# Performance work log

Hardware: AMD Instinct MI355X
Metric: run time of the kernel (lower is better)

The kernel has to match this reference:

```python
import jax, jax.numpy as jnp
import numpy as np

EMBED_DIM = 768
NUM_HEADS = 12
HEAD_DIM = EMBED_DIM // NUM_HEADS


def setup_inputs() -> dict:
    key = jax.random.key(0)
    ks = jax.random.split(key, 9)
    B, N, D = 8, 1024, EMBED_DIM
    s = 1.0 / np.sqrt(D)
    x = jax.random.normal(ks[0], (B, N, D), dtype=jnp.float32)
    Wq = jax.random.normal(ks[1], (D, D), dtype=jnp.float32) * s
    bq = jnp.zeros((D,), dtype=jnp.float32)
    Wk = jax.random.normal(ks[2], (D, D), dtype=jnp.float32) * s
    bk = jnp.zeros((D,), dtype=jnp.float32)
    Wv = jax.random.normal(ks[3], (D, D), dtype=jnp.float32) * s
    bv = jnp.zeros((D,), dtype=jnp.float32)
    Wo = jax.random.normal(ks[4], (D, D), dtype=jnp.float32) * s
    bo = jnp.zeros((D,), dtype=jnp.float32)
    return {"x": x, "Wq": Wq, "bq": bq, "Wk": Wk, "bk": bk,
            "Wv": Wv, "bv": bv, "Wo": Wo, "bo": bo}


def reference(x, Wq, bq, Wk, bk, Wv, bv, Wo, bo):
    B, N, D = x.shape
    H, Hd = NUM_HEADS, HEAD_DIM
    # torch Linear: y = x @ W.T + b
    q = (x @ Wq.T + bq).reshape(B, N, H, Hd).transpose(0, 2, 1, 3)  # [B,H,N,Hd]
    k = (x @ Wk.T + bk).reshape(B, N, H, Hd).transpose(0, 2, 1, 3)
    v = (x @ Wv.T + bv).reshape(B, N, H, Hd).transpose(0, 2, 1, 3)
    # NOTE: original scales by embed_dim**-0.5 (not head_dim)
    scale = jnp.asarray(D, x.dtype) ** -0.5
    scores = jnp.einsum('bhnd,bhmd->bhnm', q, k) * scale  # [B,H,N,N]
    attn = jax.nn.softmax(scores, axis=-1)
    out = jnp.einsum('bhnm,bhmd->bhnd', attn, v)  # dropout: identity in eval
    out = out.transpose(0, 2, 1, 3).reshape(B, N, D)
    return out @ Wo.T + bo
```

## Files before the change

kernel.cpp:

```cpp
#include <hip/hip_runtime.h>
#include <math.h>


typedef __bf16 bf16x8 __attribute__((ext_vector_type(8)));
typedef float  f32x4  __attribute__((ext_vector_type(4)));
typedef unsigned u32x2 __attribute__((ext_vector_type(2)));
typedef unsigned u32x4 __attribute__((ext_vector_type(4)));
typedef unsigned short ushort_t;

__device__ __forceinline__ unsigned short f2bf(float f) {
    unsigned u = __float_as_uint(f);
    u += 0x7fffu + ((u >> 16) & 1u);
    return (unsigned short)(u >> 16);
}
__device__ __forceinline__ unsigned pk16(unsigned short lo, unsigned short hi) {
    return (unsigned)lo | ((unsigned)hi << 16);
}

#define GLL16(g, l)                                                                        \
    __builtin_amdgcn_global_load_lds((const __attribute__((address_space(1))) void*)(g),   \
                                     (__attribute__((address_space(3))) void*)(l), 16, 0, 0)

__global__ __launch_bounds__(256)
void cast_all(const float* __restrict__ x,
              const float* __restrict__ w0, const float* __restrict__ w1,
              const float* __restrict__ w2, const float* __restrict__ w3,
              ushort_t* __restrict__ xb, ushort_t* __restrict__ wb0,
              ushort_t* __restrict__ wb1, ushort_t* __restrict__ wb2,
              ushort_t* __restrict__ wb3)
{
    const int y = blockIdx.y;
    const float* s; ushort_t* d; int n;
    switch (y) {
        case 0:  s = x;  d = xb;  n = 8192 * 768; break;
        case 1:  s = w0; d = wb0; n = 768 * 768;  break;
        case 2:  s = w1; d = wb1; n = 768 * 768;  break;
        case 3:  s = w2; d = wb2; n = 768 * 768;  break;
        default: s = w3; d = wb3; n = 768 * 768;  break;
    }
    const int i = (blockIdx.x * 256 + threadIdx.x) * 8;
    if (i >= n) return;
    const float4 f0 = *(const float4*)(s + i);
    const float4 f1 = *(const float4*)(s + i + 4);
    ushort4 p0, p1;
    p0.x = f2bf(f0.x); p0.y = f2bf(f0.y); p0.z = f2bf(f0.z); p0.w = f2bf(f0.w);
    p1.x = f2bf(f1.x); p1.y = f2bf(f1.y); p1.z = f2bf(f1.z); p1.w = f2bf(f1.w);
    *(ushort4*)(d + i)     = p0;
    *(ushort4*)(d + i + 4) = p1;
}

__device__ __forceinline__ void gemm_core_mfma(
    const ushort_t* __restrict__ A, const ushort_t* __restrict__ W,
    int m0, int n0, ushort_t* smem, f32x4 acc[4][4])
{
    ushort_t* As = smem;
    ushort_t* Ws = smem + 4096;
    const int tid = threadIdx.x;
    const int L   = tid & 63;
    const int wv  = tid >> 6;
    const int wr  = wv >> 1, wc = wv & 1;
    const int c   = L & 15,  g  = L >> 4;

    const int c0 = tid, c1 = tid + 256;
    const int qs = ((tid & 3) ^ ((tid >> 3) & 3)) * 8;
    const ushort_t* a0 = A + (size_t)(m0 + (c0 >> 2)) * 768 + qs;
    const ushort_t* a1 = A + (size_t)(m0 + (c1 >> 2)) * 768 + qs;
    const ushort_t* w0 = W + (size_t)(n0 + (c0 >> 2)) * 768 + qs;
    const ushort_t* w1 = W + (size_t)(n0 + (c1 >> 2)) * 768 + qs;
    const int sg = (g ^ ((c >> 1) & 3)) * 8;

#pragma unroll
    for (int i = 0; i < 4; ++i)
#pragma unroll
        for (int j = 0; j < 4; ++j) acc[i][j] = (f32x4){0.f, 0.f, 0.f, 0.f};

    for (int k0 = 0; k0 < 768; k0 += 32) {
        __syncthreads();
        GLL16(a0 + k0, &As[(size_t)c0 * 8]);
        GLL16(a1 + k0, &As[(size_t)c1 * 8]);
        GLL16(w0 + k0, &Ws[(size_t)c0 * 8]);
        GLL16(w1 + k0, &Ws[(size_t)c1 * 8]);
        __syncthreads();
        bf16x8 af[4], bfr[4];
#pragma unroll
        for (int i = 0; i < 4; ++i)
            af[i] = *(const bf16x8*)&As[(wr * 64 + i * 16 + c) * 32 + sg];
#pragma unroll
        for (int j = 0; j < 4; ++j)
            bfr[j] = *(const bf16x8*)&Ws[(wc * 64 + j * 16 + c) * 32 + sg];
#pragma unroll
        for (int i = 0; i < 4; ++i)
#pragma unroll
            for (int j = 0; j < 4; ++j)
                acc[i][j] = __builtin_amdgcn_mfma_f32_16x16x32_bf16(
                    af[i], bfr[j], acc[i][j], 0, 0, 0);
    }
}

__global__ __launch_bounds__(256, 3)
void gemm_qkv(const ushort_t* __restrict__ xb,
              const ushort_t* __restrict__ wqb, const ushort_t* __restrict__ wkb,
              const ushort_t* __restrict__ wvb,
              const float* __restrict__ bq, const float* __restrict__ bk,
              const float* __restrict__ bv,
              ushort_t* __restrict__ Qh, ushort_t* __restrict__ Kl,
              ushort_t* __restrict__ Vl)
{
    __shared__ ushort_t smem[14336];
    ushort_t* As  = smem;
    ushort_t* Ws0 = smem + 2048;
    ushort_t* Ws1 = smem + 6144;
    ushort_t* Ws2 = smem + 10240;

    const int tid = threadIdx.x, L = tid & 63, wv = tid >> 6;
    const int c = L & 15, g = L >> 4;
    const int n0 = blockIdx.x * 128, m0 = blockIdx.y * 64;

    const int qs = ((tid & 3) ^ ((tid >> 3) & 3)) * 8;
    const ushort_t* ap = xb  + (size_t)(m0 + (tid >> 2)) * 768 + qs;
    const ushort_t* wq = wqb + (size_t)(n0 + (tid >> 2)) * 768 + qs;
    const ushort_t* wk = wkb + (size_t)(n0 + (tid >> 2)) * 768 + qs;
    const ushort_t* wvp = wvb + (size_t)(n0 + (tid >> 2)) * 768 + qs;
    const size_t st64 = (size_t)64 * 768;
    const int sg = (g ^ ((c >> 1) & 3)) * 8;

    f32x4 acc[3][4][2];
#pragma unroll
    for (int z = 0; z < 3; ++z)
#pragma unroll
        for (int i = 0; i < 4; ++i)
#pragma unroll
            for (int j = 0; j < 2; ++j) acc[z][i][j] = (f32x4){0.f, 0.f, 0.f, 0.f};

    for (int k0 = 0; k0 < 768; k0 += 32) {
        __syncthreads();
        GLL16(ap + k0,          &As[(size_t)tid * 8]);
        GLL16(wq + k0,          &Ws0[(size_t)tid * 8]);
        GLL16(wq + st64 + k0,   &Ws0[(size_t)(tid + 256) * 8]);
        GLL16(wk + k0,          &Ws1[(size_t)tid * 8]);
        GLL16(wk + st64 + k0,   &Ws1[(size_t)(tid + 256) * 8]);
        GLL16(wvp + k0,         &Ws2[(size_t)tid * 8]);
        GLL16(wvp + st64 + k0,  &Ws2[(size_t)(tid + 256) * 8]);
        __syncthreads();
        bf16x8 af[4];
#pragma unroll
        for (int i = 0; i < 4; ++i)
            af[i] = *(const bf16x8*)&As[(i * 16 + c) * 32 + sg];
        bf16x8 bf[3][2];
        const ushort_t* wsz[3] = {Ws0, Ws1, Ws2};
#pragma unroll
        for (int z = 0; z < 3; ++z)
#pragma unroll
            for (int j = 0; j < 2; ++j)
                bf[z][j] = *(const bf16x8*)&wsz[z][(wv * 32 + j * 16 + c) * 32 + sg];
#pragma unroll
        for (int z = 0; z < 3; ++z)
#pragma unroll
            for (int i = 0; i < 4; ++i)
#pragma unroll
                for (int j = 0; j < 2; ++j)
                    acc[z][i][j] = __builtin_amdgcn_mfma_f32_16x16x32_bf16(
                        af[i], bf[z][j], acc[z][i][j], 0, 0, 0);
    }

    const int b  = m0 >> 10, nb = m0 & 1023;
    const int hcol = n0 + wv * 32;
    const int h = hcol >> 6, uh = (hcol >> 5) & 1;
    const int bh = b * 12 + h;
    ushort_t* scr = smem + wv * 2304;

    float bias2[3][2];
#pragma unroll
    for (int j = 0; j < 2; ++j) {
        bias2[0][j] = bq[hcol + j * 16 + c];
        bias2[1][j] = bk[hcol + j * 16 + c];
        bias2[2][j] = bv[hcol + j * 16 + c];
    }

    __syncthreads();

#pragma unroll
    for (int i = 0; i < 4; ++i)
#pragma unroll
        for (int j = 0; j < 2; ++j)
#pragma unroll
            for (int r = 0; r < 4; ++r)
                scr[(i * 16 + g * 4 + r) * 36 + j * 16 + c] =
                    f2bf(acc[0][i][j][r] + bias2[0][j]);
#pragma unroll
    for (int e = 0; e < 4; ++e) {
        const int slot = e * 64 + L;
        const int row = slot >> 2, ch = slot & 3;
        const u32x4 v = *(const u32x4*)&scr[row * 36 + ch * 8];
        *(u32x4*)&Qh[((size_t)bh * 1024 + nb + row) * 64 + uh * 32 + ch * 8] = v;
    }

#pragma unroll
    for (int i = 0; i < 4; ++i)
#pragma unroll
        for (int j = 0; j < 2; ++j)
#pragma unroll
            for (int r = 0; r < 4; ++r)
                scr[(i * 16 + g * 4 + r) * 36 + j * 16 + c] =
                    f2bf(acc[1][i][j][r] + bias2[1][j]);
#pragma unroll
    for (int tau = 0; tau < 4; ++tau) {
        const u32x4 v = *(const u32x4*)&scr[(tau * 16 + c) * 36 + g * 8];
        *(u32x4*)&Kl[(((size_t)bh * 64 + (nb >> 4) + tau) * 2 + uh) * 512
                     + (size_t)L * 8] = v;
    }

#pragma unroll
    for (int i = 0; i < 4; ++i)
#pragma unroll
        for (int j = 0; j < 2; ++j)
#pragma unroll
            for (int r = 0; r < 4; ++r)
                scr[(j * 16 + c) * 68 + i * 16 + g * 4 + r] =
                    f2bf(acc[2][i][j][r] + bias2[2][j]);
    const int T = nb >> 6;
#pragma unroll
    for (int t = 0; t < 4; ++t) {
        const int htl = t >> 1, u = t & 1;
        const u32x4 v = *(const u32x4*)&scr[(htl * 16 + c) * 68 + u * 32 + g * 8];
        *(u32x4*)&Vl[((((size_t)bh * 4 + uh * 2 + htl) * 16 + T) * 2 + u) * 512
                     + (size_t)L * 8] = v;
    }
}

__global__ __launch_bounds__(256, 3)
void gemm_outp(const ushort_t* __restrict__ attnb, const ushort_t* __restrict__ wob,
               const float* __restrict__ bo, float* __restrict__ out)
{
    __shared__ ushort_t smem[8192];
    const int m0 = blockIdx.y * 128, n0 = blockIdx.x * 128;
    f32x4 acc[4][4];
    gemm_core_mfma(attnb, wob, m0, n0, smem, acc);
    const int tid = threadIdx.x, L = tid & 63, wv2 = tid >> 6;
    const int wr = wv2 >> 1, wc = wv2 & 1, c = L & 15, g = L >> 4;
#pragma unroll
    for (int i = 0; i < 4; ++i) {
        const int row = m0 + wr * 64 + i * 16 + g * 4;
#pragma unroll
        for (int j = 0; j < 4; ++j) {
            const int col = n0 + wc * 64 + j * 16 + c;
            const float bsvo = bo[col];
#pragma unroll
            for (int r = 0; r < 4; ++r)
                out[(size_t)(row + r) * 768 + col] = acc[i][j][r] + bsvo;
        }
    }
}

__global__ __launch_bounds__(64, 3)
void flash_bf16(const ushort_t* __restrict__ Q, const ushort_t* __restrict__ Kl,
                const ushort_t* __restrict__ Vl, ushort_t* __restrict__ attnb)
{
    __shared__ ushort_t Ps[2][16 * 68];
    const int L = threadIdx.x;
    const int c = L & 15, g = L >> 4;
    const int bh = blockIdx.x, q0 = blockIdx.y * 32;
    const float SC2 = 0.05205954985329743f;

    const ushort_t* Qp = Q + ((size_t)bh * 1024 + q0 + c) * 64 + g * 8;
    bf16x8 qf[2][2];
    qf[0][0] = *(const bf16x8*)Qp;
    qf[0][1] = *(const bf16x8*)(Qp + 32);
    qf[1][0] = *(const bf16x8*)(Qp + 16 * 64);
    qf[1][1] = *(const bf16x8*)(Qp + 16 * 64 + 32);

    const ushort_t* Kb = Kl + (size_t)bh * 65536 + (size_t)L * 8;
    const ushort_t* Vb = Vl + (size_t)bh * 65536 + (size_t)L * 8;

    f32x4 o[2][4];
#pragma unroll
    for (int w = 0; w < 2; ++w)
#pragma unroll
        for (int ht = 0; ht < 4; ++ht) o[w][ht] = (f32x4){0.f, 0.f, 0.f, 0.f};
    float ls[2] = {0.f, 0.f};

    bf16x8 kf0[4], kf1[4];
#pragma unroll
    for (int ct = 0; ct < 4; ++ct) {
        kf0[ct] = *(const bf16x8*)(Kb + (size_t)(ct * 2 + 0) * 512);
        kf1[ct] = *(const bf16x8*)(Kb + (size_t)(ct * 2 + 1) * 512);
    }

    for (int T = 0; T < 16; ++T) {
        bf16x8 vf0[4], vf1[4];
#pragma unroll
        for (int ht = 0; ht < 4; ++ht) {
            const ushort_t* vp = Vb + (size_t)((ht * 16 + T) * 2) * 512;
            vf0[ht] = *(const bf16x8*)vp;
            vf1[ht] = *(const bf16x8*)(vp + 512);
        }
        f32x4 s[2][4];
#pragma unroll
        for (int w = 0; w < 2; ++w)
#pragma unroll
            for (int ct = 0; ct < 4; ++ct) {
                f32x4 zz = (f32x4){0.f, 0.f, 0.f, 0.f};
                zz = __builtin_amdgcn_mfma_f32_16x16x32_bf16(kf0[ct], qf[w][0], zz, 0, 0, 0);
                zz = __builtin_amdgcn_mfma_f32_16x16x32_bf16(kf1[ct], qf[w][1], zz, 0, 0, 0);
                s[w][ct] = zz;
            }
        const int Tn = (T < 15) ? T + 1 : 15;
#pragma unroll
        for (int ct = 0; ct < 4; ++ct) {
            const ushort_t* kp = Kb + (size_t)((Tn * 4 + ct) * 2) * 512;
            kf0[ct] = *(const bf16x8*)kp;
            kf1[ct] = *(const bf16x8*)(kp + 512);
        }
#pragma unroll
        for (int w = 0; w < 2; ++w) {
#pragma unroll
            for (int ct = 0; ct < 4; ++ct) {
                float p[4];
#pragma unroll
                for (int r = 0; r < 4; ++r)
                    p[r] = __builtin_amdgcn_exp2f(s[w][ct][r] * SC2);
                ls[w] += (p[0] + p[1]) + (p[2] + p[3]);
                const unsigned w01 = __builtin_amdgcn_perm(
                    __float_as_uint(p[1]), __float_as_uint(p[0]), 0x07060302u);
                const unsigned w23 = __builtin_amdgcn_perm(
                    __float_as_uint(p[3]), __float_as_uint(p[2]), 0x07060302u);
                *(u32x2*)&Ps[w][c * 68 + ct * 16 + g * 4] = (u32x2){w01, w23};
            }
        }
#pragma unroll
        for (int w = 0; w < 2; ++w) {
            const int pb = c * 68 + g * 8;
            const u32x4 pa  = *(const u32x4*)&Ps[w][pb];
            const u32x4 pbv = *(const u32x4*)&Ps[w][pb + 32];
            const bf16x8 pf0 = __builtin_bit_cast(bf16x8, pa);
            const bf16x8 pf1 = __builtin_bit_cast(bf16x8, pbv);
#pragma unroll
            for (int ht = 0; ht < 4; ++ht) {
                o[w][ht] = __builtin_amdgcn_mfma_f32_16x16x32_bf16(vf0[ht], pf0, o[w][ht], 0, 0, 0);
                o[w][ht] = __builtin_amdgcn_mfma_f32_16x16x32_bf16(vf1[ht], pf1, o[w][ht], 0, 0, 0);
            }
        }
    }

    const int b = bh / 12, h = bh % 12;
#pragma unroll
    for (int w = 0; w < 2; ++w) {
        float l = ls[w];
        l += __shfl_xor(l, 16);
        l += __shfl_xor(l, 32);
        const float inv = 1.f / l;
#pragma unroll
        for (int ht = 0; ht < 4; ++ht) {
            const unsigned w0 = pk16(f2bf(o[w][ht][0] * inv), f2bf(o[w][ht][1] * inv));
            const unsigned w1 = pk16(f2bf(o[w][ht][2] * inv), f2bf(o[w][ht][3] * inv));
            *(u32x2*)&Ps[w][c * 68 + ht * 16 + g * 4] = (u32x2){w0, w1};
        }
#pragma unroll
        for (int e = 0; e < 2; ++e) {
            const int row = e * 8 + (L >> 3);
            const int ch  = L & 7;
            const int si  = row * 68 + ch * 8;
            const u32x2 t0 = *(const u32x2*)&Ps[w][si];
            const u32x2 t1 = *(const u32x2*)&Ps[w][si + 4];
            *(u32x4*)&attnb[((size_t)(b * 1024 + q0 + w * 16 + row)) * 768 + h * 64 + ch * 8]
                = (u32x4){t0.x, t0.y, t1.x, t1.y};
        }
    }
}

extern "C" void kernel_launch(void* const* d_in, const int* in_sizes, int n_in,
                              void* d_out, int out_size, void* d_ws, size_t ws_size,
                              hipStream_t stream)
{
    const float* x  = (const float*)d_in[0];
    const float* Wq = (const float*)d_in[1];
    const float* bq = (const float*)d_in[2];
    const float* Wk = (const float*)d_in[3];
    const float* bk = (const float*)d_in[4];
    const float* Wv = (const float*)d_in[5];
    const float* bv = (const float*)d_in[6];
    const float* Wo = (const float*)d_in[7];
    const float* bo = (const float*)d_in[8];
    float* out = (float*)d_out;

    char* ws = (char*)d_ws;
    ushort_t* xb    = (ushort_t*)(ws);
    ushort_t* wqb   = (ushort_t*)(ws + 12582912);
    ushort_t* wkb   = (ushort_t*)(ws + 12582912 + 1179648);
    ushort_t* wvb   = (ushort_t*)(ws + 12582912 + 2359296);
    ushort_t* wob   = (ushort_t*)(ws + 12582912 + 3538944);
    ushort_t* Qh    = (ushort_t*)(ws + 17301504);
    ushort_t* Kl    = (ushort_t*)(ws + 29884416);
    ushort_t* Vl    = (ushort_t*)(ws + 42467328);
    ushort_t* attnb = (ushort_t*)(ws + 55050240);

    cast_all<<<dim3(3072, 5), 256, 0, stream>>>(x, Wq, Wk, Wv, Wo,
                                                xb, wqb, wkb, wvb, wob);
    gemm_qkv<<<dim3(6, 128), 256, 0, stream>>>(xb, wqb, wkb, wvb,
                                               bq, bk, bv, Qh, Kl, Vl);
    flash_bf16<<<dim3(96, 32), 64, 0, stream>>>(Qh, Kl, Vl, attnb);
    gemm_outp<<<dim3(6, 64), 256, 0, stream>>>(attnb, wob, bo, out);
}
```

Before: 196.4 us.

## Retile output projection to 64x128 blocks and double-buffer P in flash loop

The output-projection GEMM now uses 64x128 tiles with each wave owning a 64x32 strip, which doubles the grid to 768 blocks and cuts shared memory per block, aiming at better occupancy and CU fill. The flash attention loop is unrolled by two key tiles with a separate P staging buffer for each, so the write of one tile's probabilities does not have to wait on reads of the previous tile. The cost is less operand reuse per block in the GEMM (more A/W reloads) and extra LDS in the attention kernel.

```diff
diff --git a/kernel.cpp b/kernel.cpp
--- a/kernel.cpp
+++ b/kernel.cpp
@@ -47,54 +47,6 @@
     p1.x = f2bf(f1.x); p1.y = f2bf(f1.y); p1.z = f2bf(f1.z); p1.w = f2bf(f1.w);
     *(ushort4*)(d + i)     = p0;
     *(ushort4*)(d + i + 4) = p1;
-}
-
-__device__ __forceinline__ void gemm_core_mfma(
-    const ushort_t* __restrict__ A, const ushort_t* __restrict__ W,
-    int m0, int n0, ushort_t* smem, f32x4 acc[4][4])
-{
-    ushort_t* As = smem;
-    ushort_t* Ws = smem + 4096;
-    const int tid = threadIdx.x;
-    const int L   = tid & 63;
-    const int wv  = tid >> 6;
-    const int wr  = wv >> 1, wc = wv & 1;
-    const int c   = L & 15,  g  = L >> 4;
-
-    const int c0 = tid, c1 = tid + 256;
-    const int qs = ((tid & 3) ^ ((tid >> 3) & 3)) * 8;
-    const ushort_t* a0 = A + (size_t)(m0 + (c0 >> 2)) * 768 + qs;
-    const ushort_t* a1 = A + (size_t)(m0 + (c1 >> 2)) * 768 + qs;
-    const ushort_t* w0 = W + (size_t)(n0 + (c0 >> 2)) * 768 + qs;
-    const ushort_t* w1 = W + (size_t)(n0 + (c1 >> 2)) * 768 + qs;
-    const int sg = (g ^ ((c >> 1) & 3)) * 8;
-
-#pragma unroll
-    for (int i = 0; i < 4; ++i)
-#pragma unroll
-        for (int j = 0; j < 4; ++j) acc[i][j] = (f32x4){0.f, 0.f, 0.f, 0.f};
-
-    for (int k0 = 0; k0 < 768; k0 += 32) {
-        __syncthreads();
-        GLL16(a0 + k0, &As[(size_t)c0 * 8]);
-        GLL16(a1 + k0, &As[(size_t)c1 * 8]);
-        GLL16(w0 + k0, &Ws[(size_t)c0 * 8]);
-        GLL16(w1 + k0, &Ws[(size_t)c1 * 8]);
-        __syncthreads();
-        bf16x8 af[4], bfr[4];
-#pragma unroll
-        for (int i = 0; i < 4; ++i)
-            af[i] = *(const bf16x8*)&As[(wr * 64 + i * 16 + c) * 32 + sg];
-#pragma unroll
-        for (int j = 0; j < 4; ++j)
-            bfr[j] = *(const bf16x8*)&Ws[(wc * 64 + j * 16 + c) * 32 + sg];
-#pragma unroll
-        for (int i = 0; i < 4; ++i)
-#pragma unroll
-            for (int j = 0; j < 4; ++j)
-                acc[i][j] = __builtin_amdgcn_mfma_f32_16x16x32_bf16(
-                    af[i], bfr[j], acc[i][j], 0, 0, 0);
-    }
 }
 
 __global__ __launch_bounds__(256, 3)
@@ -232,18 +184,51 @@
 void gemm_outp(const ushort_t* __restrict__ attnb, const ushort_t* __restrict__ wob,
                const float* __restrict__ bo, float* __restrict__ out)
 {
-    __shared__ ushort_t smem[8192];
-    const int m0 = blockIdx.y * 128, n0 = blockIdx.x * 128;
-    f32x4 acc[4][4];
-    gemm_core_mfma(attnb, wob, m0, n0, smem, acc);
-    const int tid = threadIdx.x, L = tid & 63, wv2 = tid >> 6;
-    const int wr = wv2 >> 1, wc = wv2 & 1, c = L & 15, g = L >> 4;
+    __shared__ ushort_t smem[6144];
+    ushort_t* As = smem;
+    ushort_t* Ws = smem + 2048;
+    const int tid = threadIdx.x, L = tid & 63, wv = tid >> 6;
+    const int c = L & 15, g = L >> 4;
+    const int n0 = blockIdx.x * 128, m0 = blockIdx.y * 64;
+    const int qs = ((tid & 3) ^ ((tid >> 3) & 3)) * 8;
+    const ushort_t* ap = attnb + (size_t)(m0 + (tid >> 2)) * 768 + qs;
+    const ushort_t* wp = wob   + (size_t)(n0 + (tid >> 2)) * 768 + qs;
+    const size_t st64 = (size_t)64 * 768;
+    const int sg = (g ^ ((c >> 1) & 3)) * 8;
+
+    f32x4 acc[4][2];
+#pragma unroll
+    for (int i = 0; i < 4; ++i)
+#pragma unroll
+        for (int j = 0; j < 2; ++j) acc[i][j] = (f32x4){0.f, 0.f, 0.f, 0.f};
+
+    for (int k0 = 0; k0 < 768; k0 += 32) {
+        __syncthreads();
+        GLL16(ap + k0,        &As[(size_t)tid * 8]);
+        GLL16(wp + k0,        &Ws[(size_t)tid * 8]);
+        GLL16(wp + st64 + k0, &Ws[(size_t)(tid + 256) * 8]);
+        __syncthreads();
+        bf16x8 af[4], bf[2];
+#pragma unroll
+        for (int i = 0; i < 4; ++i)
+            af[i] = *(const bf16x8*)&As[(i * 16 + c) * 32 + sg];
+#pragma unroll
+        for (int j = 0; j < 2; ++j)
+            bf[j] = *(const bf16x8*)&Ws[(wv * 32 + j * 16 + c) * 32 + sg];
+#pragma unroll
+        for (int i = 0; i < 4; ++i)
+#pragma unroll
+            for (int j = 0; j < 2; ++j)
+                acc[i][j] = __builtin_amdgcn_mfma_f32_16x16x32_bf16(
+                    af[i], bf[j], acc[i][j], 0, 0, 0);
+    }
+
 #pragma unroll
     for (int i = 0; i < 4; ++i) {
-        const int row = m0 + wr * 64 + i * 16 + g * 4;
-#pragma unroll
-        for (int j = 0; j < 4; ++j) {
-            const int col = n0 + wc * 64 + j * 16 + c;
+        const int row = m0 + i * 16 + g * 4;
+#pragma unroll
+        for (int j = 0; j < 2; ++j) {
+            const int col = n0 + wv * 32 + j * 16 + c;
             const float bsvo = bo[col];
 #pragma unroll
             for (int r = 0; r < 4; ++r)
@@ -256,7 +241,7 @@
 void flash_bf16(const ushort_t* __restrict__ Q, const ushort_t* __restrict__ Kl,
                 const ushort_t* __restrict__ Vl, ushort_t* __restrict__ attnb)
 {
-    __shared__ ushort_t Ps[2][16 * 68];
+    __shared__ ushort_t Ps[2][2][16 * 68];
     const int L = threadIdx.x;
     const int c = L & 15, g = L >> 4;
     const int bh = blockIdx.x, q0 = blockIdx.y * 32;
@@ -286,58 +271,62 @@
         kf1[ct] = *(const bf16x8*)(Kb + (size_t)(ct * 2 + 1) * 512);
     }
 
-    for (int T = 0; T < 16; ++T) {
-        bf16x8 vf0[4], vf1[4];
-#pragma unroll
-        for (int ht = 0; ht < 4; ++ht) {
-            const ushort_t* vp = Vb + (size_t)((ht * 16 + T) * 2) * 512;
-            vf0[ht] = *(const bf16x8*)vp;
-            vf1[ht] = *(const bf16x8*)(vp + 512);
-        }
-        f32x4 s[2][4];
-#pragma unroll
-        for (int w = 0; w < 2; ++w)
+    for (int T0 = 0; T0 < 16; T0 += 2) {
+#pragma unroll
+        for (int p = 0; p < 2; ++p) {
+            const int T = T0 + p;
+            bf16x8 vf0[4], vf1[4];
+#pragma unroll
+            for (int ht = 0; ht < 4; ++ht) {
+                const ushort_t* vp = Vb + (size_t)((ht * 16 + T) * 2) * 512;
+                vf0[ht] = *(const bf16x8*)vp;
+                vf1[ht] = *(const bf16x8*)(vp + 512);
+            }
+            f32x4 s[2][4];
+#pragma unroll
+            for (int w = 0; w < 2; ++w)
+#pragma unroll
+                for (int ct = 0; ct < 4; ++ct) {
+                    f32x4 zz = (f32x4){0.f, 0.f, 0.f, 0.f};
+                    zz = __builtin_amdgcn_mfma_f32_16x16x32_bf16(kf0[ct], qf[w][0], zz, 0, 0, 0);
+                    zz = __builtin_amdgcn_mfma_f32_16x16x32_bf16(kf1[ct], qf[w][1], zz, 0, 0, 0);
+                    s[w][ct] = zz;
+                }
+            const int Tn = (T < 15) ? T + 1 : 15;
 #pragma unroll
             for (int ct = 0; ct < 4; ++ct) {
-                f32x4 zz = (f32x4){0.f, 0.f, 0.f, 0.f};
-                zz = __builtin_amdgcn_mfma_f32_16x16x32_bf16(kf0[ct], qf[w][0], zz, 0, 0, 0);
-                zz = __builtin_amdgcn_mfma_f32_16x16x32_bf16(kf1[ct], qf[w][1], zz, 0, 0, 0);
-                s[w][ct] = zz;
+                const ushort_t* kp = Kb + (size_t)((Tn * 4 + ct) * 2) * 512;
+                kf0[ct] = *(const bf16x8*)kp;
+                kf1[ct] = *(const bf16x8*)(kp + 512);
             }
-        const int Tn = (T < 15) ? T + 1 : 15;
-#pragma unroll
-        for (int ct = 0; ct < 4; ++ct) {
-            const ushort_t* kp = Kb + (size_t)((Tn * 4 + ct) * 2) * 512;
-            kf0[ct] = *(const bf16x8*)kp;
-            kf1[ct] = *(const bf16x8*)(kp + 512);
-        }
-#pragma unroll
-        for (int w = 0; w < 2; ++w) {
-#pragma unroll
-            for (int ct = 0; ct < 4; ++ct) {
-                float p[4];
-#pragma unroll
-                for (int r = 0; r < 4; ++r)
-                    p[r] = __builtin_amdgcn_exp2f(s[w][ct][r] * SC2);
-                ls[w] += (p[0] + p[1]) + (p[2] + p[3]);
-                const unsigned w01 = __builtin_amdgcn_perm(
-                    __float_as_uint(p[1]), __float_as_uint(p[0]), 0x07060302u);
-                const unsigned w23 = __builtin_amdgcn_perm(
-                    __float_as_uint(p[3]), __float_as_uint(p[2]), 0x07060302u);
-                *(u32x2*)&Ps[w][c * 68 + ct * 16 + g * 4] = (u32x2){w01, w23};
+#pragma unroll
+            for (int w = 0; w < 2; ++w) {
+#pragma unroll
+                for (int ct = 0; ct < 4; ++ct) {
+                    float pv[4];
+#pragma unroll
+                    for (int r = 0; r < 4; ++r)
+                        pv[r] = __builtin_amdgcn_exp2f(s[w][ct][r] * SC2);
+                    ls[w] += (pv[0] + pv[1]) + (pv[2] + pv[3]);
+                    const unsigned w01 = __builtin_amdgcn_perm(
+                        __float_as_uint(pv[1]), __float_as_uint(pv[0]), 0x07060302u);
+                    const unsigned w23 = __builtin_amdgcn_perm(
+                        __float_as_uint(pv[3]), __float_as_uint(pv[2]), 0x07060302u);
+                    *(u32x2*)&Ps[p][w][c * 68 + ct * 16 + g * 4] = (u32x2){w01, w23};
+                }
             }
-        }
-#pragma unroll
-        for (int w = 0; w < 2; ++w) {
-            const int pb = c * 68 + g * 8;
-            const u32x4 pa  = *(const u32x4*)&Ps[w][pb];
-            const u32x4 pbv = *(const u32x4*)&Ps[w][pb + 32];
-            const bf16x8 pf0 = __builtin_bit_cast(bf16x8, pa);
-            const bf16x8 pf1 = __builtin_bit_cast(bf16x8, pbv);
-#pragma unroll
-            for (int ht = 0; ht < 4; ++ht) {
-                o[w][ht] = __builtin_amdgcn_mfma_f32_16x16x32_bf16(vf0[ht], pf0, o[w][ht], 0, 0, 0);
-                o[w][ht] = __builtin_amdgcn_mfma_f32_16x16x32_bf16(vf1[ht], pf1, o[w][ht], 0, 0, 0);
+#pragma unroll
+            for (int w = 0; w < 2; ++w) {
+                const int pb = c * 68 + g * 8;
+                const u32x4 pa  = *(const u32x4*)&Ps[p][w][pb];
+                const u32x4 pbv = *(const u32x4*)&Ps[p][w][pb + 32];
+                const bf16x8 pf0 = __builtin_bit_cast(bf16x8, pa);
+                const bf16x8 pf1 = __builtin_bit_cast(bf16x8, pbv);
+#pragma unroll
+                for (int ht = 0; ht < 4; ++ht) {
+                    o[w][ht] = __builtin_amdgcn_mfma_f32_16x16x32_bf16(vf0[ht], pf0, o[w][ht], 0, 0, 0);
+                    o[w][ht] = __builtin_amdgcn_mfma_f32_16x16x32_bf16(vf1[ht], pf1, o[w][ht], 0, 0, 0);
+                }
             }
         }
     }
@@ -353,15 +342,15 @@
         for (int ht = 0; ht < 4; ++ht) {
             const unsigned w0 = pk16(f2bf(o[w][ht][0] * inv), f2bf(o[w][ht][1] * inv));
             const unsigned w1 = pk16(f2bf(o[w][ht][2] * inv), f2bf(o[w][ht][3] * inv));
-            *(u32x2*)&Ps[w][c * 68 + ht * 16 + g * 4] = (u32x2){w0, w1};
+            *(u32x2*)&Ps[0][w][c * 68 + ht * 16 + g * 4] = (u32x2){w0, w1};
         }
 #pragma unroll
         for (int e = 0; e < 2; ++e) {
             const int row = e * 8 + (L >> 3);
             const int ch  = L & 7;
             const int si  = row * 68 + ch * 8;
-            const u32x2 t0 = *(const u32x2*)&Ps[w][si];
-            const u32x2 t1 = *(const u32x2*)&Ps[w][si + 4];
+            const u32x2 t0 = *(const u32x2*)&Ps[0][w][si];
+            const u32x2 t1 = *(const u32x2*)&Ps[0][w][si + 4];
             *(u32x4*)&attnb[((size_t)(b * 1024 + q0 + w * 16 + row)) * 768 + h * 64 + ch * 8]
                 = (u32x4){t0.x, t0.y, t1.x, t1.y};
         }
@@ -399,5 +388,5 @@
     gemm_qkv<<<dim3(6, 128), 256, 0, stream>>>(xb, wqb, wkb, wvb,
                                                bq, bk, bv, Qh, Kl, Vl);
     flash_bf16<<<dim3(96, 32), 64, 0, stream>>>(Qh, Kl, Vl, attnb);
-    gemm_outp<<<dim3(6, 64), 256, 0, stream>>>(attnb, wob, bo, out);
-}
+    gemm_outp<<<dim3(6, 128), 256, 0, stream>>>(attnb, wob, bo, out);
+}
```

Result: no change. 197.8 us (+0.7%).
